# Performance work log

Measured on AMD Instinct MI355X. Metric: run time of the kernel, lower is better.

Reference implementation:

```python
import jax, jax.numpy as jnp
import numpy as np

DIM = 1024
NUM_HEADS = 16
HEAD_DIM = DIM // NUM_HEADS  # 64
LATENT = 128
Q_RANK = 256
B, S = 4, 2048


def setup_inputs() -> dict:
    key = jax.random.key(0)
    ks = jax.random.split(key, 12)
    w = lambda k, shape: jax.random.normal(k, shape, dtype=jnp.float32) * 0.02
    x = jax.random.normal(ks[0], (B, S, DIM), dtype=jnp.float32)
    mask = jnp.tril(jnp.ones((S, S), dtype=jnp.int32))[None, None, :, :]  # causal [1,1,S,S]
    return {
        "x": x,
        "mask": mask,
        "w_kvc": w(ks[1], (DIM, LATENT)),   "b_kvc": jnp.zeros((LATENT,), jnp.float32),
        "w_kvu": w(ks[2], (LATENT, 2 * DIM)), "b_kvu": jnp.zeros((2 * DIM,), jnp.float32),
        "w_qc":  w(ks[3], (DIM, Q_RANK)),   "b_qc": jnp.zeros((Q_RANK,), jnp.float32),
        "w_qu":  w(ks[4], (Q_RANK, DIM)),   "b_qu": jnp.zeros((DIM,), jnp.float32),
        "w_o":   w(ks[5], (DIM, DIM)),      "b_o": jnp.zeros((DIM,), jnp.float32),
    }


def reference(x, mask, w_kvc, b_kvc, w_kvu, b_kvu, w_qc, b_qc, w_qu, b_qu, w_o, b_o):
    b, s, _ = x.shape
    # low-rank KV path
    kv_latent = x @ w_kvc + b_kvc                      # [B,S,latent]
    kv_up = kv_latent @ w_kvu + b_kvu                  # [B,S,2*dim]
    K, V = jnp.split(kv_up, 2, axis=-1)                # each [B,S,dim]
    # low-rank Q path
    Q = (x @ w_qc + b_qc) @ w_qu + b_qu                # [B,S,dim]

    def split_heads(t):  # [B,S,dim] -> [B,H,S,hd]
        return t.reshape(b, s, NUM_HEADS, HEAD_DIM).transpose(0, 2, 1, 3)

    Qh, Kh, Vh = split_heads(Q), split_heads(K), split_heads(V)
    scores = jnp.einsum("bhsd,bhtd->bhst", Qh, Kh) / np.sqrt(HEAD_DIM).astype(np.float32)
    scores = jnp.where(mask == 0, jnp.float32(-1e9), scores)
    attn = jax.nn.softmax(scores, axis=-1)
    ctx = jnp.einsum("bhst,bhtd->bhsd", attn, Vh)      # [B,H,S,hd]
    ctx = ctx.transpose(0, 2, 1, 3).reshape(b, s, DIM)
    return ctx @ w_o + b_o
```

## Files before the change

### kernel.cpp

```cpp
#include <hip/hip_runtime.h>

typedef __attribute__((ext_vector_type(8))) short short8;
typedef __attribute__((ext_vector_type(4))) float f32x4;

#define DIM 1024
#define NH 16
#define HD 64
#define LAT 128
#define QR 256
#define NCAT (LAT + QR)
#define BB 4
#define SS 2048
#define BS (BB * SS)

#define SCALE_LOG2E 0.18033688011112042f

__device__ __forceinline__ unsigned short f2b(float f) {
  unsigned int u = __builtin_bit_cast(unsigned int, f);
  u += 0x7FFFu + ((u >> 16) & 1u);
  return (unsigned short)(u >> 16);
}
__device__ __forceinline__ float b2f(unsigned short h) {
  unsigned int u = ((unsigned int)h) << 16;
  return __builtin_bit_cast(float, u);
}
__device__ __forceinline__ unsigned int pack_bf16_pair(float f0, float f1) {
  unsigned int u0 = __builtin_bit_cast(unsigned int, f0) + 0x8000u;
  unsigned int u1 = __builtin_bit_cast(unsigned int, f1) + 0x8000u;
  return __builtin_amdgcn_perm(u1, u0, 0x07060302u);
}
__device__ __forceinline__ void gll16(const unsigned short* g, unsigned short* l) {
  __builtin_amdgcn_global_load_lds(
      (const __attribute__((address_space(1))) unsigned int*)g,
      (__attribute__((address_space(3))) unsigned int*)l, 16, 0, 0);
}

__global__ __launch_bounds__(256) void cvt_x(const float* __restrict__ in,
                                             unsigned short* __restrict__ out, int n4) {
  int i = blockIdx.x * 256 + threadIdx.x;
  if (i >= n4) return;
  f32x4 v = ((const f32x4*)in)[i];
  ushort4 o;
  o.x = f2b(v[0]); o.y = f2b(v[1]); o.z = f2b(v[2]); o.w = f2b(v[3]);
  ((ushort4*)out)[i] = o;
}

__global__ __launch_bounds__(256) void prep_weights(
    const float* __restrict__ w_kvc, const float* __restrict__ w_qc,
    const float* __restrict__ w_kvu, const float* __restrict__ w_qu,
    const float* __restrict__ w_o, const float* __restrict__ b_kvc,
    const float* __restrict__ b_qc, unsigned short* __restrict__ wcatT,
    unsigned short* __restrict__ wkvuT, unsigned short* __restrict__ wquT,
    unsigned short* __restrict__ woT, float* __restrict__ bias_cat) {
  __shared__ unsigned short T[64 * 72];
  const int id = blockIdx.x;
  const int tid = threadIdx.x;
  if (id >= 480) {
    if (tid < LAT) bias_cat[tid] = b_kvc[tid];
    else bias_cat[tid] = b_qc[tid - LAT];
    if (tid < 128) bias_cat[tid + 256] = b_qc[tid + 128];
    return;
  }
  const float* in; unsigned short* out; int K, N, tile;
  if (id < 32)       { in = w_kvc; out = wcatT;                       K = DIM; N = LAT;     tile = id; }
  else if (id < 96)  { in = w_qc;  out = wcatT + (size_t)LAT * DIM;   K = DIM; N = QR;      tile = id - 32; }
  else if (id < 160) { in = w_kvu; out = wkvuT;                       K = LAT; N = 2 * DIM; tile = id - 96; }
  else if (id < 224) { in = w_qu;  out = wquT;                        K = QR;  N = DIM;     tile = id - 160; }
  else               { in = w_o;   out = woT;                         K = DIM; N = DIM;     tile = id - 224; }
  const int ktiles = K >> 6;
  const int k0 = (tile % ktiles) * 64, n0 = (tile / ktiles) * 64;
  {
    const int r = tid >> 2, cq = (tid & 3) * 16;
#pragma unroll
    for (int j = 0; j < 4; ++j) {
      f32x4 v = *(const f32x4*)(in + (size_t)(k0 + r) * N + n0 + cq + j * 4);
      ushort4 o;
      o.x = f2b(v[0]); o.y = f2b(v[1]); o.z = f2b(v[2]); o.w = f2b(v[3]);
      *(ushort4*)(T + r * 72 + cq + j * 4) = o;
    }
  }
  __syncthreads();
#pragma unroll
  for (int s = 0; s < 2; ++s) {
    int idx = tid + s * 256;
    int nr = idx >> 3, kg = (idx & 7) * 8;
    short8 o;
#pragma unroll
    for (int i = 0; i < 8; i++) o[i] = T[(kg + i) * 72 + nr];
    *(short8*)(out + (size_t)(n0 + nr) * K + k0 + kg) = o;
  }
}

__global__ __launch_bounds__(256, 4) void gemm_lds(const unsigned short* __restrict__ A,
                                                   const unsigned short* __restrict__ WT,
                                                   const float* __restrict__ bias,
                                                   float* __restrict__ outF,
                                                   unsigned short* __restrict__ outB,
                                                   unsigned short* __restrict__ vtOut,
                                                   int N, int K, int lda, int ldout,
                                                   float scale, int nblk) {
  __shared__ unsigned short gsm[17408];
  const int tid = threadIdx.x;
  const int wave = tid >> 6, lane = tid & 63;
  const int ln = lane & 15, quad = lane >> 4;
  const int chunk = nblk >> 3;
  const int sw = (blockIdx.x & 7) * chunk + (blockIdx.x >> 3);
  const int nwx = N >> 7;
  const int bx = sw % nwx, by = sw / nwx;
  const int m0 = by * 128, n0 = bx * 128;
  const int wm = (wave >> 1) * 64, wn = (wave & 1) * 64;

  const int srow = wave * 32 + (lane >> 2);
  const int scol = (lane & 3) * 8;
  const unsigned short* Ag = A + (size_t)(m0 + srow) * lda + scol;
  const unsigned short* Bg = WT + (size_t)(n0 + srow) * K + scol;

  f32x4 acc[4][4];
#pragma unroll
  for (int i = 0; i < 4; i++)
#pragma unroll
    for (int j = 0; j < 4; j++) acc[i][j] = (f32x4){0.f, 0.f, 0.f, 0.f};

#define STAGE(buf, kk)                                                        \
  {                                                                           \
    unsigned short* Al = gsm + (buf) * 4096 + wave * 1024;                    \
    unsigned short* Bl = gsm + 8192 + (buf) * 4096 + wave * 1024;             \
    gll16(Ag + (kk), Al);                                                     \
    gll16(Ag + (size_t)16 * lda + (kk), Al + 512);                            \
    gll16(Bg + (kk), Bl);                                                     \
    gll16(Bg + (size_t)16 * K + (kk), Bl + 512);                              \
  }

  STAGE(0, 0);
  __syncthreads();
  const int T = K >> 5;
  int cur = 0;
  for (int t = 0; t < T; ++t) {
    if (t + 1 < T) STAGE(cur ^ 1, (t + 1) * 32);
    const unsigned short* Ab = gsm + cur * 4096;
    const unsigned short* Bb = gsm + 8192 + cur * 4096;
    short8 af[4], bf[4];
#pragma unroll
    for (int i = 0; i < 4; i++) {
      af[i] = *(const short8*)(Ab + (wm + i * 16 + ln) * 32 + quad * 8);
      bf[i] = *(const short8*)(Bb + (wn + i * 16 + ln) * 32 + quad * 8);
    }
#pragma unroll
    for (int mi = 0; mi < 4; mi++)
#pragma unroll
      for (int ni = 0; ni < 4; ni++)
        acc[mi][ni] =
            __builtin_amdgcn_mfma_f32_16x16x32_bf16(af[mi], bf[ni], acc[mi][ni], 0, 0, 0);
    __syncthreads();
    cur ^= 1;
  }
#undef STAGE

  if (vtOut && n0 >= DIM) {
#pragma unroll
    for (int mi = 0; mi < 4; mi++) {
      const int s = wm + mi * 16 + quad * 4;
#pragma unroll
      for (int ni = 0; ni < 4; ni++) {
        const int d = wn + ni * 16 + ln;
        const float bv = bias[n0 + d];
#pragma unroll
        for (int r = 0; r < 4; r++)
          gsm[d * 136 + s + r] = f2b(acc[mi][ni][r] + bv);
      }
    }
    __syncthreads();
    const int d0 = n0 - DIM, bb = m0 >> 11, s0l = m0 & (SS - 1);
#pragma unroll
    for (int t = 0; t < 8; ++t) {
      int idx = tid + t * 256;
      int dr = idx >> 4, cs = (idx & 15) * 8;
      short8 v = *(const short8*)(gsm + dr * 136 + cs);
      *(short8*)(vtOut + (size_t)(bb * DIM + d0 + dr) * SS + s0l + cs) = v;
    }
    return;
  }

#pragma unroll
  for (int mi = 0; mi < 4; mi++) {
    const int row = m0 + wm + mi * 16 + quad * 4;
#pragma unroll
    for (int ni = 0; ni < 4; ni++) {
      const int col = n0 + wn + ni * 16 + ln;
      const float bv = bias[col];
#pragma unroll
      for (int r = 0; r < 4; r++) {
        float v = (acc[mi][ni][r] + bv) * scale;
        size_t o = (size_t)(row + r) * ldout + col;
        if (outF) outF[o] = v;
        if (outB) outB[o] = f2b(v);
      }
    }
  }
}

__global__ __launch_bounds__(256, 4) void attn_mfma(const unsigned short* __restrict__ Qb,
                                                    const unsigned short* __restrict__ KVb,
                                                    const unsigned short* __restrict__ VTb,
                                                    unsigned short* __restrict__ ctxB) {
  __shared__ unsigned short smem[12288];
  unsigned short* Ks = smem;
  unsigned short* Vts = smem + 4096;
  unsigned short* Ps = smem + 8192;
  const int tid = threadIdx.x;
  const int wave = tid >> 6, lane = tid & 63;
  const int ln = lane & 15, quad = lane >> 4;
  const int hw = blockIdx.x;
  const int xcd = hw & 7, slot = hw >> 3;
  const int grp = xcd * 8 + (slot >> 4);
  const int pair = slot & 15;
  const int h = grp & 15, b = grp >> 4;
  const int tA = pair, tB = 31 - pair;
  const int s0A = tA * 64, s0B = tB * 64;
  const int ktmaxB = tB;
  const int qminA = s0A + wave * 16, qmaxA = qminA + 15;
  const int qminB = s0B + wave * 16, qmaxB = qminB + 15;

  short8 qfA[2], qfB[2];
  {
    const unsigned short* qa =
        Qb + (size_t)(b * SS + s0A + wave * 16 + ln) * DIM + h * HD + quad * 8;
    qfA[0] = *(const short8*)qa;
    qfA[1] = *(const short8*)(qa + 32);
    const unsigned short* qb2 =
        Qb + (size_t)(b * SS + s0B + wave * 16 + ln) * DIM + h * HD + quad * 8;
    qfB[0] = *(const short8*)qb2;
    qfB[1] = *(const short8*)(qb2 + 32);
  }

  f32x4 ocA[4], ocB[4];
  float lpA = 0.f, lpB = 0.f;
#pragma unroll
  for (int i = 0; i < 4; i++) {
    ocA[i] = (f32x4){0.f, 0.f, 0.f, 0.f};
    ocB[i] = (f32x4){0.f, 0.f, 0.f, 0.f};
  }

  unsigned short* Pw = Ps + wave * (16 * 64);
  const int swz = (ln & 7) << 3;

  const int srow = tid >> 3, sc8 = (tid & 7) * 8;
  const int ssc = sc8 ^ ((srow & 7) << 3);

  const unsigned short* kptr =
      KVb + (size_t)(b * SS + srow) * (2 * DIM) + h * HD + sc8;
  const unsigned short* vptr = VTb + (size_t)(b * DIM + h * HD + srow) * SS + sc8;
  const size_t kstep = (size_t)64 * 2 * DIM;
  const size_t krow32 = (size_t)32 * 2 * DIM;
  const size_t vrow32 = (size_t)32 * SS;

  short8 kreg0 = *(const short8*)kptr;
  short8 kreg1 = *(const short8*)(kptr + krow32);
  short8 vreg0 = *(const short8*)vptr;
  short8 vreg1 = *(const short8*)(vptr + vrow32);

  for (int kt = 0; kt <= ktmaxB; ++kt) {
    __syncthreads();
    *(short8*)(Ks + srow * 64 + ssc) = kreg0;
    *(short8*)(Ks + (srow + 32) * 64 + ssc) = kreg1;
    *(short8*)(Vts + srow * 64 + ssc) = vreg0;
    *(short8*)(Vts + (srow + 32) * 64 + ssc) = vreg1;
    __syncthreads();
    if (kt < ktmaxB) {
      kptr += kstep; vptr += 64;
      kreg0 = *(const short8*)kptr;
      kreg1 = *(const short8*)(kptr + krow32);
      vreg0 = *(const short8*)vptr;
      vreg1 = *(const short8*)(vptr + vrow32);
    }

    const int k0g = kt * 64;

    auto stream = [&](const short8* qf, f32x4* oc, float& lp, const int qminw,
                      const int qmaxw) {
      if (k0g > qmaxw) return;
      const bool needmask = (k0g + 63 > qminw);

      f32x4 sacc[4];
#pragma unroll
      for (int nt = 0; nt < 4; nt++) sacc[nt] = (f32x4){0.f, 0.f, 0.f, 0.f};
      __builtin_amdgcn_s_setprio(1);
#pragma unroll
      for (int kc = 0; kc < 2; kc++) {
        const int rc = (kc * 32 + quad * 8) ^ swz;
#pragma unroll
        for (int nt = 0; nt < 4; nt++) {
          if (k0g + nt * 16 > qmaxw) continue;
          short8 kfrag = *(const short8*)(Ks + (nt * 16 + ln) * 64 + rc);
          sacc[nt] =
              __builtin_amdgcn_mfma_f32_16x16x32_bf16(kfrag, qf[kc], sacc[nt], 0, 0, 0);
        }
      }
      __builtin_amdgcn_s_setprio(0);

      const int qg = qminw + ln;
      float lt = 0.f;
      if (!needmask) {
#pragma unroll
        for (int nt = 0; nt < 4; nt++) {
          float p0 = __builtin_exp2f(sacc[nt][0]);
          float p1 = __builtin_exp2f(sacc[nt][1]);
          float p2 = __builtin_exp2f(sacc[nt][2]);
          float p3 = __builtin_exp2f(sacc[nt][3]);
          uint2 pw;
          pw.x = pack_bf16_pair(p0, p1);
          pw.y = pack_bf16_pair(p2, p3);
          *(uint2*)(Pw + ln * 64 + ((nt * 16 + quad * 4) ^ swz)) = pw;
          lt += (p0 + p1) + (p2 + p3);
        }
      } else {
#pragma unroll
        for (int nt = 0; nt < 4; nt++) {
          const int base = k0g + nt * 16 + quad * 4;
          float pe[4];
#pragma unroll
          for (int r = 0; r < 4; r++) {
            float p = __builtin_exp2f(sacc[nt][r]);
            if (base + r > qg) p = 0.f;
            pe[r] = p;
          }
          uint2 pw;
          pw.x = pack_bf16_pair(pe[0], pe[1]);
          pw.y = pack_bf16_pair(pe[2], pe[3]);
          *(uint2*)(Pw + ln * 64 + ((nt * 16 + quad * 4) ^ swz)) = pw;
          lt += (pe[0] + pe[1]) + (pe[2] + pe[3]);
        }
      }
      lp += lt;

      __builtin_amdgcn_s_setprio(1);
#pragma unroll
      for (int kc = 0; kc < 2; kc++) {
        if (k0g + kc * 32 > qmaxw) continue;
        const int rc = (kc * 32 + quad * 8) ^ swz;
        short8 pfrag = *(const short8*)(Pw + ln * 64 + rc);
#pragma unroll
        for (int dt = 0; dt < 4; dt++) {
          short8 vfrag = *(const short8*)(Vts + (dt * 16 + ln) * 64 + rc);
          oc[dt] =
              __builtin_amdgcn_mfma_f32_16x16x32_bf16(pfrag, vfrag, oc[dt], 0, 0, 0);
        }
      }
      __builtin_amdgcn_s_setprio(0);
    };

    stream(qfA, ocA, lpA, qminA, qmaxA);
    stream(qfB, ocB, lpB, qminB, qmaxB);
  }

  lpA += __shfl_xor(lpA, 16, 64);
  lpA += __shfl_xor(lpA, 32, 64);
  lpB += __shfl_xor(lpB, 16, 64);
  lpB += __shfl_xor(lpB, 32, 64);
  float liA[4], liB[4];
#pragma unroll
  for (int r = 0; r < 4; r++) {
    liA[r] = 1.f / __shfl(lpA, quad * 4 + r, 64);
    liB[r] = 1.f / __shfl(lpB, quad * 4 + r, 64);
  }

  __syncthreads();
#pragma unroll
  for (int r = 0; r < 4; r++) {
#pragma unroll
    for (int dt = 0; dt < 4; dt++)
      smem[(wave * 16 + quad * 4 + r) * 72 + dt * 16 + ln] = f2b(ocA[dt][r] * liA[r]);
  }
  __syncthreads();
#pragma unroll
  for (int t = 0; t < 2; ++t) {
    int idx = tid + t * 256;
    int row = idx >> 3, c = idx & 7;
    short8 v = *(const short8*)(smem + row * 72 + c * 8);
    *(short8*)(ctxB + (size_t)(b * SS + s0A + row) * DIM + h * HD + c * 8) = v;
  }
  __syncthreads();
#pragma unroll
  for (int r = 0; r < 4; r++) {
#pragma unroll
    for (int dt = 0; dt < 4; dt++)
      smem[(wave * 16 + quad * 4 + r) * 72 + dt * 16 + ln] = f2b(ocB[dt][r] * liB[r]);
  }
  __syncthreads();
#pragma unroll
  for (int t = 0; t < 2; ++t) {
    int idx = tid + t * 256;
    int row = idx >> 3, c = idx & 7;
    short8 v = *(const short8*)(smem + row * 72 + c * 8);
    *(short8*)(ctxB + (size_t)(b * SS + s0B + row) * DIM + h * HD + c * 8) = v;
  }
}

extern "C" void kernel_launch(void* const* d_in, const int* in_sizes, int n_in,
                              void* d_out, int out_size, void* d_ws, size_t ws_size,
                              hipStream_t stream) {
  const float* x     = (const float*)d_in[0];
  const float* w_kvc = (const float*)d_in[2];
  const float* b_kvc = (const float*)d_in[3];
  const float* w_kvu = (const float*)d_in[4];
  const float* b_kvu = (const float*)d_in[5];
  const float* w_qc  = (const float*)d_in[6];
  const float* b_qc  = (const float*)d_in[7];
  const float* w_qu  = (const float*)d_in[8];
  const float* b_qu  = (const float*)d_in[9];
  const float* w_o   = (const float*)d_in[10];
  const float* b_o   = (const float*)d_in[11];
  float* out = (float*)d_out;

  unsigned short* xb     = (unsigned short*)d_ws;
  unsigned short* wcatT  = xb + (size_t)BS * DIM;
  unsigned short* wkvuT  = wcatT + (size_t)NCAT * DIM;
  unsigned short* wquT   = wkvuT + (size_t)LAT * 2 * DIM;
  unsigned short* woT    = wquT + (size_t)QR * DIM;
  unsigned short* kvqlat = woT + (size_t)DIM * DIM;
  unsigned short* kvup   = kvqlat + (size_t)BS * NCAT;
  unsigned short* Qbuf   = kvup + (size_t)BS * 2 * DIM;
  unsigned short* ctx    = Qbuf + (size_t)BS * DIM;
  float* bias_cat        = (float*)(ctx + (size_t)BS * DIM);

  cvt_x<<<(BS * DIM / 4 + 255) / 256, 256, 0, stream>>>(x, xb, BS * DIM / 4);
  prep_weights<<<481, 256, 0, stream>>>(w_kvc, w_qc, w_kvu, w_qu, w_o, b_kvc, b_qc,
                                        wcatT, wkvuT, wquT, woT, bias_cat);

  gemm_lds<<<dim3(BS / 128 * (NCAT / 128)), 256, 0, stream>>>(
      xb, wcatT, bias_cat, nullptr, kvqlat, nullptr, NCAT, DIM, DIM, NCAT, 1.0f,
      BS / 128 * (NCAT / 128));
  unsigned short* VT = xb;
  gemm_lds<<<dim3(BS / 128 * (2 * DIM / 128)), 256, 0, stream>>>(
      kvqlat, wkvuT, b_kvu, nullptr, kvup, VT, 2 * DIM, LAT, NCAT, 2 * DIM, 1.0f,
      BS / 128 * (2 * DIM / 128));
  gemm_lds<<<dim3(BS / 128 * (DIM / 128)), 256, 0, stream>>>(
      kvqlat + LAT, wquT, b_qu, nullptr, Qbuf, nullptr, DIM, QR, NCAT, DIM, SCALE_LOG2E,
      BS / 128 * (DIM / 128));
  attn_mfma<<<dim3(32 * NH * BB / 2), 256, 0, stream>>>(Qbuf, kvup, VT, ctx);
  gemm_lds<<<dim3(BS / 128 * (DIM / 128)), 256, 0, stream>>>(
      ctx, woT, b_o, out, nullptr, nullptr, DIM, DIM, DIM, DIM, 1.0f,
      BS / 128 * (DIM / 128));
}
```

Measured before the change: 254.8 us.

## Deepen GEMM LDS pipeline to four stages with XOR-swizzled LDS layout

Replaces the double-buffered LDS staging in the bf16 GEMM kernel with a four-buffer ring that keeps three tiles of global-to-LDS loads in flight, using explicit vmcnt waits and one barrier per iteration instead of two syncthreads. It also XOR-swizzles the column chunk per row on both the load and read sides to reduce LDS bank conflicts. LDS use roughly doubles and launch bounds drop to two blocks per SM, which lowers occupancy in exchange for deeper latency hiding.

```diff
diff --git a/kernel.cpp b/kernel.cpp
--- a/kernel.cpp
+++ b/kernel.cpp
@@ -91,7 +91,7 @@
   }
 }
 
-__global__ __launch_bounds__(256, 4) void gemm_lds(const unsigned short* __restrict__ A,
+__global__ __launch_bounds__(256, 2) void gemm_lds(const unsigned short* __restrict__ A,
                                                    const unsigned short* __restrict__ WT,
                                                    const float* __restrict__ bias,
                                                    float* __restrict__ outF,
@@ -99,7 +99,7 @@
                                                    unsigned short* __restrict__ vtOut,
                                                    int N, int K, int lda, int ldout,
                                                    float scale, int nblk) {
-  __shared__ unsigned short gsm[17408];
+  __shared__ unsigned short gsm[32768];
   const int tid = threadIdx.x;
   const int wave = tid >> 6, lane = tid & 63;
   const int ln = lane & 15, quad = lane >> 4;
@@ -110,10 +110,10 @@
   const int m0 = by * 128, n0 = bx * 128;
   const int wm = (wave >> 1) * 64, wn = (wave & 1) * 64;
 
-  const int srow = wave * 32 + (lane >> 2);
-  const int scol = (lane & 3) * 8;
-  const unsigned short* Ag = A + (size_t)(m0 + srow) * lda + scol;
-  const unsigned short* Bg = WT + (size_t)(n0 + srow) * K + scol;
+  const int sr = lane >> 2;
+  const int scg = (lane & 3) ^ (sr & 3);
+  const unsigned short* Ag = A + (size_t)(m0 + wave * 32 + sr) * lda + scg * 8;
+  const unsigned short* Bg = WT + (size_t)(n0 + wave * 32 + sr) * K + scg * 8;
 
   f32x4 acc[4][4];
 #pragma unroll
@@ -124,26 +124,34 @@
 #define STAGE(buf, kk)                                                        \
   {                                                                           \
     unsigned short* Al = gsm + (buf) * 4096 + wave * 1024;                    \
-    unsigned short* Bl = gsm + 8192 + (buf) * 4096 + wave * 1024;             \
+    unsigned short* Bl = gsm + 16384 + (buf) * 4096 + wave * 1024;            \
     gll16(Ag + (kk), Al);                                                     \
     gll16(Ag + (size_t)16 * lda + (kk), Al + 512);                            \
     gll16(Bg + (kk), Bl);                                                     \
     gll16(Bg + (size_t)16 * K + (kk), Bl + 512);                              \
   }
 
+  const int T = K >> 5;
   STAGE(0, 0);
-  __syncthreads();
-  const int T = K >> 5;
-  int cur = 0;
+  STAGE(1, 32);
+  STAGE(2, 64);
+
+  const int rc = (quad ^ (ln & 3)) * 8;
   for (int t = 0; t < T; ++t) {
-    if (t + 1 < T) STAGE(cur ^ 1, (t + 1) * 32);
-    const unsigned short* Ab = gsm + cur * 4096;
-    const unsigned short* Bb = gsm + 8192 + cur * 4096;
+    const int rem = T - 1 - t;
+    if (rem >= 2)      asm volatile("s_waitcnt vmcnt(8)" ::: "memory");
+    else if (rem == 1) asm volatile("s_waitcnt vmcnt(4)" ::: "memory");
+    else               asm volatile("s_waitcnt vmcnt(0)" ::: "memory");
+    asm volatile("s_waitcnt lgkmcnt(0)" ::: "memory");
+    __builtin_amdgcn_s_barrier();
+    if (t + 3 < T) STAGE((t + 3) & 3, (t + 3) * 32);
+    const unsigned short* Ab = gsm + (t & 3) * 4096;
+    const unsigned short* Bb = gsm + 16384 + (t & 3) * 4096;
     short8 af[4], bf[4];
 #pragma unroll
     for (int i = 0; i < 4; i++) {
-      af[i] = *(const short8*)(Ab + (wm + i * 16 + ln) * 32 + quad * 8);
-      bf[i] = *(const short8*)(Bb + (wn + i * 16 + ln) * 32 + quad * 8);
+      af[i] = *(const short8*)(Ab + (wm + i * 16 + ln) * 32 + rc);
+      bf[i] = *(const short8*)(Bb + (wn + i * 16 + ln) * 32 + rc);
     }
 #pragma unroll
     for (int mi = 0; mi < 4; mi++)
@@ -151,12 +159,11 @@
       for (int ni = 0; ni < 4; ni++)
         acc[mi][ni] =
             __builtin_amdgcn_mfma_f32_16x16x32_bf16(af[mi], bf[ni], acc[mi][ni], 0, 0, 0);
+  }
+#undef STAGE
+
+  if (vtOut && n0 >= DIM) {
     __syncthreads();
-    cur ^= 1;
-  }
-#undef STAGE
-
-  if (vtOut && n0 >= DIM) {
 #pragma unroll
     for (int mi = 0; mi < 4; mi++) {
       const int s = wm + mi * 16 + quad * 4;
```

New measurement: 256.2 us. No clear change (+0.5%).
